# Optimization experiments

Hardware: AMD Instinct MI355X
Metric: run time of the kernel (lower is better)

## Reference

```python
import jax, jax.numpy as jnp
import numpy as np

DIM_IN = 256
DIM_OUT = 256
HEADS = 4
B, H, W = 8, 64, 64
S_Q, S_KV = 1, 2
EPS = 1e-5


def _dw_proj(x, dw, g, bta, mu, var, pw, stride):
    # depthwise 3x3 conv (groups=C) + BatchNorm (inference) + 1x1 pointwise conv
    C = x.shape[1]
    y = jax.lax.conv_general_dilated(
        x, dw, (stride, stride), [(1, 1), (1, 1)],
        dimension_numbers=('NCHW', 'OIHW', 'NCHW'), feature_group_count=C)
    inv = g / jnp.sqrt(var + EPS)
    y = (y - mu[None, :, None, None]) * inv[None, :, None, None] + bta[None, :, None, None]
    return jnp.einsum('bchw,oc->bohw', y, pw)


def setup_inputs() -> dict:
    key = jax.random.key(0)
    ks = jax.random.split(key, 16)
    f = lambda k, s: jax.random.normal(k, s, jnp.float32) * 0.05
    inp = {'x': jax.random.normal(ks[0], (B, DIM_IN, H, W), jnp.float32)}
    for i, nm in enumerate(['q', 'k', 'v']):
        inp[f'dw_{nm}'] = f(ks[1 + i], (DIM_IN, 1, 3, 3))
        inp[f'g_{nm}'] = jnp.ones((DIM_IN,), jnp.float32)
        inp[f'b_{nm}'] = jnp.zeros((DIM_IN,), jnp.float32)
        inp[f'm_{nm}'] = f(ks[4 + i], (DIM_IN,))
        inp[f'v_{nm}'] = jax.random.uniform(ks[7 + i], (DIM_IN,), jnp.float32, 0.5, 1.5)
        inp[f'pw_{nm}'] = f(ks[10 + i], (DIM_OUT, DIM_IN))
    inp['proj_w'] = f(ks[13], (DIM_OUT, DIM_OUT))
    inp['proj_b'] = f(ks[14], (DIM_OUT,))
    return inp


def reference(x, dw_q, g_q, b_q, m_q, v_q, pw_q,
              dw_k, g_k, b_k, m_k, v_k, pw_k,
              dw_v, g_v, b_v, m_v, v_v, pw_v,
              proj_w, proj_b):
    b, _, h, w = x.shape
    d = DIM_OUT // HEADS
    q = _dw_proj(x, dw_q, g_q, b_q, m_q, v_q, pw_q, S_Q)    # [b,C,h,w]
    k = _dw_proj(x, dw_k, g_k, b_k, m_k, v_k, pw_k, S_KV)   # [b,C,h/2,w/2]
    v = _dw_proj(x, dw_v, g_v, b_v, m_v, v_v, pw_v, S_KV)

    def to_heads(t):
        bb, c, hh, ww = t.shape
        # 'b c h w -> b (h w) c' then 'b t (h d) -> b h t d' (head-major channel split)
        return t.reshape(bb, HEADS, d, hh * ww).transpose(0, 1, 3, 2)  # [b,H,t,d]

    qh, kh, vh = to_heads(q), to_heads(k), to_heads(v)
    scale = DIM_OUT ** (-0.5)  # note: scales by dim_out, not head_dim (faithful)
    attn = jax.nn.softmax(jnp.einsum('bhld,bhtd->bhlt', qh, kh) * scale, axis=-1)
    out = jnp.einsum('bhlt,bhtd->bhld', attn, vh)           # [b,H,l,d]
    # 'b h (x y) d -> b (h d) x y'
    out = out.transpose(0, 1, 3, 2).reshape(b, HEADS * d, h, w)
    out = jnp.einsum('bchw,oc->bohw', out, proj_w) + proj_b[None, :, None, None]
    return out
```

## Files before the change

kernel.cpp:

```cpp
#include <hip/hip_runtime.h>

#define B_     8
#define C_     256
#define H_     64
#define W_     64
#define HEADS_ 4
#define DH_    64
#define TQ_    4096
#define TKV_   1024
#define EPS_   1e-5f
#define SCALE_ 0.0625f

typedef __attribute__((ext_vector_type(8))) short short8;
typedef __attribute__((ext_vector_type(4))) float f32x4;

#define MFMA(a, b, c) __builtin_amdgcn_mfma_f32_16x16x32_bf16((a), (b), (c), 0, 0, 0)

static __device__ __forceinline__ unsigned short f2bf(float x) {
    unsigned u = __float_as_uint(x);
    u += 0x7fff + ((u >> 16) & 1);
    return (unsigned short)(u >> 16);
}
static __device__ __forceinline__ float bf2f(unsigned short h) {
    return __uint_as_float(((unsigned)h) << 16);
}
#define GLOAD16(gp, lp) __builtin_amdgcn_global_load_lds(                      \
    (const __attribute__((address_space(1))) void*)(gp),                       \
    (__attribute__((address_space(3))) void*)(lp), 16, 0, 0)

__global__ __launch_bounds__(256)
void w2bf4_kernel(const float* __restrict__ w0, const float* __restrict__ w1,
                  const float* __restrict__ w2, const float* __restrict__ w3,
                  unsigned short* __restrict__ h0, unsigned short* __restrict__ l0,
                  unsigned short* __restrict__ h1, unsigned short* __restrict__ l1,
                  unsigned short* __restrict__ h2, unsigned short* __restrict__ l2,
                  unsigned short* __restrict__ h3, unsigned short* __restrict__ l3) {
    int m = blockIdx.y;
    const float* wm = (m == 0) ? w0 : (m == 1) ? w1 : (m == 2) ? w2 : w3;
    unsigned short* whi = (m == 0) ? h0 : (m == 1) ? h1 : (m == 2) ? h2 : h3;
    unsigned short* wlo = (m == 0) ? l0 : (m == 1) ? l1 : (m == 2) ? l2 : l3;
    int idx = (blockIdx.x * 256 + threadIdx.x) * 4;
    const float4 v4 = *(const float4*)&wm[idx];
    float vv[4] = {v4.x, v4.y, v4.z, v4.w};
    unsigned short hh[4], ll[4];
    #pragma unroll
    for (int j = 0; j < 4; ++j) { hh[j] = f2bf(vv[j]); ll[j] = f2bf(vv[j] - bf2f(hh[j])); }
    *(ushort4*)&whi[idx] = make_ushort4(hh[0], hh[1], hh[2], hh[3]);
    *(ushort4*)&wlo[idx] = make_ushort4(ll[0], ll[1], ll[2], ll[3]);
}

__global__ __launch_bounds__(256)
void dwbn3_kernel(const float* __restrict__ x,
                  const float* __restrict__ dwq, const float* __restrict__ gq,
                  const float* __restrict__ bq,  const float* __restrict__ mq,
                  const float* __restrict__ vq,  float* __restrict__ yq,
                  const float* __restrict__ dwk, const float* __restrict__ gk,
                  const float* __restrict__ bk,  const float* __restrict__ mk,
                  const float* __restrict__ vk,  float* __restrict__ yk,
                  const float* __restrict__ dwv, const float* __restrict__ gv,
                  const float* __restrict__ bv,  const float* __restrict__ mv,
                  const float* __restrict__ vv,  float* __restrict__ yv) {
    int bid = blockIdx.x;
    const float *dw, *g, *bet, *mu, *var;
    float* y;
    int stride, Ho, Wo, base;
    if (bid < 32768) {
        dw = dwq; g = gq; bet = bq; mu = mq; var = vq; y = yq;
        stride = 1; Ho = 64; Wo = 64; base = 0;
    } else if (bid < 40960) {
        dw = dwk; g = gk; bet = bk; mu = mk; var = vk; y = yk;
        stride = 2; Ho = 32; Wo = 32; base = 32768;
    } else {
        dw = dwv; g = gv; bet = bv; mu = mv; var = vv; y = yv;
        stride = 2; Ho = 32; Wo = 32; base = 40960;
    }
    int idx = (bid - base) * 256 + threadIdx.x;
    int ow = idx % Wo;
    int t  = idx / Wo;
    int oh = t % Ho; t /= Ho;
    int c  = t % C_;
    int b  = t / C_;
    const float* xp = x + ((size_t)(b * C_ + c)) * H_ * W_;
    const float* wp = dw + c * 9;
    int ih0 = oh * stride - 1, iw0 = ow * stride - 1;
    float acc = 0.f;
    #pragma unroll
    for (int kh = 0; kh < 3; ++kh) {
        int ih = ih0 + kh;
        if (ih < 0 || ih >= H_) continue;
        #pragma unroll
        for (int kw = 0; kw < 3; ++kw) {
            int iw = iw0 + kw;
            if (iw < 0 || iw >= W_) continue;
            acc = fmaf(xp[ih * W_ + iw], wp[kh * 3 + kw], acc);
        }
    }
    float inv = g[c] * __frsqrt_rn(var[c] + EPS_);
    y[idx] = (acc - mu[c]) * inv + bet[c];
}

template<int IN_BF16, int OUT_MODE>
__global__ __launch_bounds__(256, 2)
void pw_mfma(const unsigned short* __restrict__ whi, const unsigned short* __restrict__ wlo,
             const float* __restrict__ yf32,
             const unsigned short* __restrict__ yhi, const unsigned short* __restrict__ ylo,
             unsigned short* __restrict__ ohi, unsigned short* __restrict__ olo,
             float* __restrict__ of32, const float* __restrict__ bias, int Np) {
    __shared__ unsigned short Ah[64 * 64], Al[64 * 64];
    __shared__ unsigned short Bh[64 * 64], Bl[64 * 64];
    __shared__ float scr[64 * 64];

    const int tid = threadIdx.x;
    const int l = tid & 63, w = tid >> 6;
    const int g = l >> 4, ln = l & 15;
    const int pbase = blockIdx.x * 64;
    const int obase = blockIdx.y * 64;
    const int b = blockIdx.z;

    f32x4 acc[4];
    #pragma unroll
    for (int f = 0; f < 4; ++f) acc[f] = (f32x4){0.f, 0.f, 0.f, 0.f};

    for (int c0 = 0; c0 < C_; c0 += 64) {
        #pragma unroll
        for (int ii = 0; ii < 4; ++ii) {
            int ch = w * 4 + ii;
            const unsigned short* src = (ch < 8) ? whi : wlo;
            unsigned short* dst = (ch < 8) ? Ah : Al;
            int i = ch & 7;
            size_t ge = (size_t)(obase + i * 8 + (l >> 3)) * C_ + c0 +
                        (((l & 7) ^ ((l >> 3) & 7)) * 8);
            GLOAD16(src + ge, dst + i * 512);
        }
        if constexpr (IN_BF16) {
            #pragma unroll
            for (int ii = 0; ii < 4; ++ii) {
                int ch = w * 4 + ii;
                const unsigned short* src = (ch < 8) ? yhi : ylo;
                unsigned short* dst = (ch < 8) ? Bh : Bl;
                int i = ch & 7;
                size_t ge = ((size_t)b * Np + pbase + i * 8 + (l >> 3)) * C_ + c0 +
                            (((l & 7) ^ ((l >> 3) & 7)) * 8);
                GLOAD16(src + ge, dst + i * 512);
            }
        } else {
            #pragma unroll
            for (int pass = 0; pass < 4; ++pass) {
                int idx = tid + pass * 256;
                int cr = idx >> 4, p4 = (idx & 15) * 4;
                *(float4*)&scr[cr * 64 + p4] =
                    *(const float4*)&yf32[(size_t)b * C_ * Np + (size_t)(c0 + cr) * Np + pbase + p4];
            }
        }
        __syncthreads();
        if constexpr (!IN_BF16) {
            int p = tid & 63, cq = tid >> 6;
            #pragma unroll
            for (int jj = 0; jj < 4; ++jj) {
                unsigned short hh[4], ll[4];
                #pragma unroll
                for (int j = 0; j < 4; ++j) {
                    float v = scr[(cq * 16 + jj * 4 + j) * 64 + p];
                    hh[j] = f2bf(v); ll[j] = f2bf(v - bf2f(hh[j]));
                }
                int cl = cq * 16 + jj * 4;
                int e = p * 64 + (((cl >> 3) ^ (p & 7)) * 8) + (cl & 7);
                *(ushort4*)&Bh[e] = make_ushort4(hh[0], hh[1], hh[2], hh[3]);
                *(ushort4*)&Bl[e] = make_ushort4(ll[0], ll[1], ll[2], ll[3]);
            }
            __syncthreads();
        }
        #pragma unroll
        for (int kh = 0; kh < 2; ++kh) {
            int gc = kh * 4 + g;
            int ea = (16 * w + ln) * 64 + ((gc ^ (ln & 7)) * 8);
            short8 ah = *(const short8*)&Ah[ea];
            short8 al = *(const short8*)&Al[ea];
            #pragma unroll
            for (int f = 0; f < 4; ++f) {
                int p = f * 16 + ln;
                int eb = p * 64 + ((gc ^ (p & 7)) * 8);
                short8 bh = *(const short8*)&Bh[eb];
                short8 bl = *(const short8*)&Bl[eb];
                acc[f] = MFMA(ah, bh, acc[f]);
                acc[f] = MFMA(ah, bl, acc[f]);
                acc[f] = MFMA(al, bh, acc[f]);
            }
        }
        __syncthreads();
    }

    if constexpr (OUT_MODE == 0) {
        #pragma unroll
        for (int f = 0; f < 4; ++f) {
            int p = f * 16 + ln;
            #pragma unroll
            for (int r = 0; r < 4; ++r) {
                int o = 16 * w + 4 * g + r;
                scr[p * 64 + (o ^ (4 * (p & 7)))] = acc[f][r];
            }
        }
        __syncthreads();
        int p = tid & 63, oq = tid >> 6;
        #pragma unroll
        for (int jj = 0; jj < 4; ++jj) {
            unsigned short hh[4], ll[4];
            #pragma unroll
            for (int j = 0; j < 4; ++j) {
                float v = scr[p * 64 + ((oq * 16 + jj * 4 + j) ^ (4 * (p & 7)))];
                hh[j] = f2bf(v); ll[j] = f2bf(v - bf2f(hh[j]));
            }
            size_t ge = ((size_t)b * Np + pbase + p) * C_ + obase + oq * 16 + jj * 4;
            *(ushort4*)&ohi[ge] = make_ushort4(hh[0], hh[1], hh[2], hh[3]);
            *(ushort4*)&olo[ge] = make_ushort4(ll[0], ll[1], ll[2], ll[3]);
        }
    } else if constexpr (OUT_MODE == 1) {
        #pragma unroll
        for (int f = 0; f < 4; ++f) {
            int p = pbase + f * 16 + ln;
            #pragma unroll
            for (int r = 0; r < 4; ++r) {
                int o = obase + 16 * w + 4 * g + r;
                size_t ge = ((size_t)b * C_ + o) * Np + p;
                float v = acc[f][r];
                unsigned short hh = f2bf(v);
                ohi[ge] = hh; olo[ge] = f2bf(v - bf2f(hh));
            }
        }
    } else {
        float bv[4];
        #pragma unroll
        for (int r = 0; r < 4; ++r) bv[r] = bias[obase + 16 * w + 4 * g + r];
        #pragma unroll
        for (int f = 0; f < 4; ++f) {
            int p = pbase + f * 16 + ln;
            #pragma unroll
            for (int r = 0; r < 4; ++r) {
                int o = obase + 16 * w + 4 * g + r;
                of32[((size_t)b * C_ + o) * Np + p] = acc[f][r] + bv[r];
            }
        }
    }
}

__global__ __launch_bounds__(256, 2)
void attn_mfma(const unsigned short* __restrict__ qhi, const unsigned short* __restrict__ qlo,
               const unsigned short* __restrict__ khi, const unsigned short* __restrict__ klo,
               const unsigned short* __restrict__ vhi, const unsigned short* __restrict__ vlo,
               unsigned short* __restrict__ ohi, unsigned short* __restrict__ olo) {
    __shared__ unsigned short Kh[64 * 64], Kl[64 * 64];
    __shared__ unsigned short Vh[64 * 64], Vl[64 * 64];
    __shared__ unsigned short Ph[64 * 64], Pl[64 * 64];

    const int tid = threadIdx.x, l = tid & 63, w = tid >> 6;
    const int g = l >> 4, ln = l & 15;
    const int qbase = blockIdx.x * 64;
    const int h = blockIdx.y, b = blockIdx.z;

    short8 qh[2], ql[2];
    {
        size_t base = ((size_t)b * TQ_ + qbase + 16 * w + ln) * C_ + h * DH_ + g * 8;
        qh[0] = *(const short8*)&qhi[base];
        qh[1] = *(const short8*)&qhi[base + 32];
        ql[0] = *(const short8*)&qlo[base];
        ql[1] = *(const short8*)&qlo[base + 32];
    }
    f32x4 oacc[4];
    float m_run[4], l_run[4];
    #pragma unroll
    for (int f = 0; f < 4; ++f) oacc[f] = (f32x4){0.f, 0.f, 0.f, 0.f};
    #pragma unroll
    for (int r = 0; r < 4; ++r) { m_run[r] = -1e30f; l_run[r] = 0.f; }

    for (int kt = 0; kt < TKV_; kt += 64) {
        {
            const unsigned short* src = (w == 0) ? khi : (w == 1) ? klo : (w == 2) ? vhi : vlo;
            unsigned short* dst = (w == 0) ? Kh : (w == 1) ? Kl : (w == 2) ? Vh : Vl;
            int swz = ((l & 7) ^ ((l >> 3) & 7)) * 8;
            if (w < 2) {
                size_t base = ((size_t)b * TKV_ + kt) * C_ + h * DH_;
                #pragma unroll
                for (int i = 0; i < 8; ++i)
                    GLOAD16(src + base + (size_t)(i * 8 + (l >> 3)) * C_ + swz, dst + i * 512);
            } else {
                size_t base = ((size_t)b * C_ + h * DH_) * TKV_ + kt;
                #pragma unroll
                for (int i = 0; i < 8; ++i)
                    GLOAD16(src + base + (size_t)(i * 8 + (l >> 3)) * TKV_ + swz, dst + i * 512);
            }
        }
        __syncthreads();

        f32x4 sacc[4];
        #pragma unroll
        for (int f = 0; f < 4; ++f) sacc[f] = (f32x4){0.f, 0.f, 0.f, 0.f};
        #pragma unroll
        for (int kh = 0; kh < 2; ++kh) {
            #pragma unroll
            for (int f = 0; f < 4; ++f) {
                int row = f * 16 + ln;
                int e = row * 64 + (((g + 4 * kh) ^ (ln & 7)) * 8);
                short8 bh = *(const short8*)&Kh[e];
                short8 bl = *(const short8*)&Kl[e];
                sacc[f] = MFMA(qh[kh], bh, sacc[f]);
                sacc[f] = MFMA(qh[kh], bl, sacc[f]);
                sacc[f] = MFMA(ql[kh], bh, sacc[f]);
            }
        }
        #pragma unroll
        for (int r = 0; r < 4; ++r) {
            float mm = fmaxf(fmaxf(sacc[0][r], sacc[1][r]), fmaxf(sacc[2][r], sacc[3][r]));
            #pragma unroll
            for (int off = 1; off < 16; off <<= 1) mm = fmaxf(mm, __shfl_xor(mm, off, 16));
            float mnew = fmaxf(m_run[r], mm * SCALE_);
            float corr = __expf(m_run[r] - mnew);
            float pv[4], rs = 0.f;
            #pragma unroll
            for (int f = 0; f < 4; ++f) { pv[f] = __expf(sacc[f][r] * SCALE_ - mnew); rs += pv[f]; }
            #pragma unroll
            for (int off = 1; off < 16; off <<= 1) rs += __shfl_xor(rs, off, 16);
            l_run[r] = l_run[r] * corr + rs;
            m_run[r] = mnew;
            #pragma unroll
            for (int f = 0; f < 4; ++f) oacc[f][r] *= corr;
            int q = 16 * w + 4 * g + r;
            #pragma unroll
            for (int f = 0; f < 4; ++f) {
                unsigned short hh = f2bf(pv[f]);
                int e = q * 64 + (((f * 2 + (ln >> 3)) ^ (q & 7)) * 8) + (ln & 7);
                Ph[e] = hh;
                Pl[e] = f2bf(pv[f] - bf2f(hh));
            }
        }
        __syncthreads();

        #pragma unroll
        for (int kvh = 0; kvh < 2; ++kvh) {
            int qr = 16 * w + ln;
            int pe = qr * 64 + (((kvh * 4 + g) ^ (qr & 7)) * 8);
            short8 ph = *(const short8*)&Ph[pe];
            short8 pl = *(const short8*)&Pl[pe];
            #pragma unroll
            for (int f = 0; f < 4; ++f) {
                int row = f * 16 + ln;
                int e = row * 64 + (((g + 4 * kvh) ^ (ln & 7)) * 8);
                short8 bh = *(const short8*)&Vh[e];
                short8 bl = *(const short8*)&Vl[e];
                oacc[f] = MFMA(ph, bh, oacc[f]);
                oacc[f] = MFMA(ph, bl, oacc[f]);
                oacc[f] = MFMA(pl, bh, oacc[f]);
            }
        }
        __syncthreads();
    }

    float inv[4];
    #pragma unroll
    for (int r = 0; r < 4; ++r) inv[r] = 1.f / l_run[r];
    #pragma unroll
    for (int f = 0; f < 4; ++f) {
        #pragma unroll
        for (int r = 0; r < 4; ++r) {
            float v = oacc[f][r] * inv[r];
            size_t ge = ((size_t)b * TQ_ + qbase + 16 * w + 4 * g + r) * C_ + h * DH_ + f * 16 + ln;
            unsigned short hh = f2bf(v);
            ohi[ge] = hh; olo[ge] = f2bf(v - bf2f(hh));
        }
    }
}

extern "C" void kernel_launch(void* const* d_in, const int* in_sizes, int n_in,
                              void* d_out, int out_size, void* d_ws, size_t ws_size,
                              hipStream_t stream) {
    const float* x     = (const float*)d_in[0];
    const float* dw_q  = (const float*)d_in[1];
    const float* g_q   = (const float*)d_in[2];
    const float* b_q   = (const float*)d_in[3];
    const float* m_q   = (const float*)d_in[4];
    const float* v_q   = (const float*)d_in[5];
    const float* pw_q  = (const float*)d_in[6];
    const float* dw_k  = (const float*)d_in[7];
    const float* g_k   = (const float*)d_in[8];
    const float* b_k   = (const float*)d_in[9];
    const float* m_k   = (const float*)d_in[10];
    const float* v_k   = (const float*)d_in[11];
    const float* pw_k  = (const float*)d_in[12];
    const float* dw_v  = (const float*)d_in[13];
    const float* g_v   = (const float*)d_in[14];
    const float* b_v   = (const float*)d_in[15];
    const float* m_v   = (const float*)d_in[16];
    const float* v_v   = (const float*)d_in[17];
    const float* pw_v  = (const float*)d_in[18];
    const float* projw = (const float*)d_in[19];
    const float* projb = (const float*)d_in[20];
    float* out = (float*)d_out;

    const size_t NQ = (size_t)B_ * TQ_ * C_;
    const size_t NK = (size_t)B_ * TKV_ * C_;
    const size_t NW = (size_t)C_ * C_;
    char* wsb = (char*)d_ws;
    float* yq = (float*)wsb;
    unsigned short* o_hi = (unsigned short*)wsb;
    unsigned short* o_lo = o_hi + NQ;
    size_t off = NQ * 4;
    float* yk = (float*)(wsb + off); off += NK * 4;
    float* yv = (float*)(wsb + off); off += NK * 4;
    unsigned short* q_hi = (unsigned short*)(wsb + off); off += NQ * 2;
    unsigned short* q_lo = (unsigned short*)(wsb + off); off += NQ * 2;
    unsigned short* k_hi = (unsigned short*)(wsb + off); off += NK * 2;
    unsigned short* k_lo = (unsigned short*)(wsb + off); off += NK * 2;
    unsigned short* v_hi = (unsigned short*)(wsb + off); off += NK * 2;
    unsigned short* v_lo = (unsigned short*)(wsb + off); off += NK * 2;
    unsigned short* wq_hi = (unsigned short*)(wsb + off); off += NW * 2;
    unsigned short* wq_lo = (unsigned short*)(wsb + off); off += NW * 2;
    unsigned short* wk_hi = (unsigned short*)(wsb + off); off += NW * 2;
    unsigned short* wk_lo = (unsigned short*)(wsb + off); off += NW * 2;
    unsigned short* wv_hi = (unsigned short*)(wsb + off); off += NW * 2;
    unsigned short* wv_lo = (unsigned short*)(wsb + off); off += NW * 2;
    unsigned short* wp_hi = (unsigned short*)(wsb + off); off += NW * 2;
    unsigned short* wp_lo = (unsigned short*)(wsb + off); off += NW * 2;

    w2bf4_kernel<<<dim3(64, 4), 256, 0, stream>>>(
        pw_q, pw_k, pw_v, projw,
        wq_hi, wq_lo, wk_hi, wk_lo, wv_hi, wv_lo, wp_hi, wp_lo);
    dwbn3_kernel<<<49152, 256, 0, stream>>>(
        x,
        dw_q, g_q, b_q, m_q, v_q, yq,
        dw_k, g_k, b_k, m_k, v_k, yk,
        dw_v, g_v, b_v, m_v, v_v, yv);
    pw_mfma<0, 0><<<dim3(TQ_ / 64, 4, B_), 256, 0, stream>>>(
        wq_hi, wq_lo, yq, nullptr, nullptr, q_hi, q_lo, nullptr, nullptr, TQ_);
    pw_mfma<0, 0><<<dim3(TKV_ / 64, 4, B_), 256, 0, stream>>>(
        wk_hi, wk_lo, yk, nullptr, nullptr, k_hi, k_lo, nullptr, nullptr, TKV_);
    pw_mfma<0, 1><<<dim3(TKV_ / 64, 4, B_), 256, 0, stream>>>(
        wv_hi, wv_lo, yv, nullptr, nullptr, v_hi, v_lo, nullptr, nullptr, TKV_);
    attn_mfma<<<dim3(TQ_ / 64, HEADS_, B_), 256, 0, stream>>>(
        q_hi, q_lo, k_hi, k_lo, v_hi, v_lo, o_hi, o_lo);
    pw_mfma<1, 2><<<dim3(TQ_ / 64, 4, B_), 256, 0, stream>>>(
        wp_hi, wp_lo, nullptr, o_hi, o_lo, nullptr, nullptr, out, projb, TQ_);
}
```

Measured before the change: 424.2 us.

## Double-buffer K/V tiles in attention and skip softmax rescale below a threshold

The attention kernel now double-buffers the K/V LDS tiles. It issues the async global-to-LDS load of the next tile right after the barrier, so the copy overlaps with the current tile's MFMA work, and it drops the trailing per-iteration barrier. The online softmax only rescales the running max and accumulators when some row's new tile max exceeds the stored max by more than a threshold, decided per 16-lane group with a ballot. The per-row sum is kept per lane and reduced by shuffles once at the end, instead of on every tile. The price is double the K/V LDS footprint, which may limit occupancy, plus unnormalised exponentials that can reach about e^8 before a rescale.

```diff
diff --git a/kernel.cpp b/kernel.cpp
--- a/kernel.cpp
+++ b/kernel.cpp
@@ -10,6 +10,7 @@
 #define TKV_   1024
 #define EPS_   1e-5f
 #define SCALE_ 0.0625f
+#define THR_   8.0f
 
 typedef __attribute__((ext_vector_type(8))) short short8;
 typedef __attribute__((ext_vector_type(4))) float f32x4;
@@ -248,8 +249,8 @@
                const unsigned short* __restrict__ khi, const unsigned short* __restrict__ klo,
                const unsigned short* __restrict__ vhi, const unsigned short* __restrict__ vlo,
                unsigned short* __restrict__ ohi, unsigned short* __restrict__ olo) {
-    __shared__ unsigned short Kh[64 * 64], Kl[64 * 64];
-    __shared__ unsigned short Vh[64 * 64], Vl[64 * 64];
+    __shared__ unsigned short Kh[2 * 64 * 64], Kl[2 * 64 * 64];
+    __shared__ unsigned short Vh[2 * 64 * 64], Vl[2 * 64 * 64];
     __shared__ unsigned short Ph[64 * 64], Pl[64 * 64];
 
     const int tid = threadIdx.x, l = tid & 63, w = tid >> 6;
@@ -266,30 +267,32 @@
         ql[1] = *(const short8*)&qlo[base + 32];
     }
     f32x4 oacc[4];
-    float m_run[4], l_run[4];
+    float m_run[4], lpart[4];
     #pragma unroll
     for (int f = 0; f < 4; ++f) oacc[f] = (f32x4){0.f, 0.f, 0.f, 0.f};
     #pragma unroll
-    for (int r = 0; r < 4; ++r) { m_run[r] = -1e30f; l_run[r] = 0.f; }
-
-    for (int kt = 0; kt < TKV_; kt += 64) {
-        {
-            const unsigned short* src = (w == 0) ? khi : (w == 1) ? klo : (w == 2) ? vhi : vlo;
-            unsigned short* dst = (w == 0) ? Kh : (w == 1) ? Kl : (w == 2) ? Vh : Vl;
-            int swz = ((l & 7) ^ ((l >> 3) & 7)) * 8;
-            if (w < 2) {
-                size_t base = ((size_t)b * TKV_ + kt) * C_ + h * DH_;
-                #pragma unroll
-                for (int i = 0; i < 8; ++i)
-                    GLOAD16(src + base + (size_t)(i * 8 + (l >> 3)) * C_ + swz, dst + i * 512);
-            } else {
-                size_t base = ((size_t)b * C_ + h * DH_) * TKV_ + kt;
-                #pragma unroll
-                for (int i = 0; i < 8; ++i)
-                    GLOAD16(src + base + (size_t)(i * 8 + (l >> 3)) * TKV_ + swz, dst + i * 512);
-            }
-        }
+    for (int r = 0; r < 4; ++r) { m_run[r] = -1e30f; lpart[r] = 0.f; }
+
+    const int swz = ((l & 7) ^ ((l >> 3) & 7)) * 8;
+    const unsigned short* ssrc = (w == 0) ? khi : (w == 1) ? klo : (w == 2) ? vhi : vlo;
+    unsigned short* sdst0 = (w == 0) ? Kh : (w == 1) ? Kl : (w == 2) ? Vh : Vl;
+    const size_t sstride = (w < 2) ? (size_t)C_ : (size_t)TKV_;
+    const size_t sgbase  = (w < 2) ? ((size_t)b * TKV_) * C_ + h * DH_
+                                   : ((size_t)b * C_ + h * DH_) * TKV_;
+    auto STAGE = [&](int sel, int kt) {
+        size_t ko = (w < 2) ? (size_t)kt * C_ : (size_t)kt;
+        unsigned short* dst = sdst0 + sel * 4096;
+        #pragma unroll
+        for (int i = 0; i < 8; ++i)
+            GLOAD16(ssrc + sgbase + ko + (size_t)(i * 8 + (l >> 3)) * sstride + swz,
+                    dst + i * 512);
+    };
+
+    STAGE(0, 0);
+    for (int it = 0; it < TKV_ / 64; ++it) {
+        const int cur = it & 1, so = cur * 4096;
         __syncthreads();
+        if (it + 1 < TKV_ / 64) STAGE(cur ^ 1, (it + 1) * 64);
 
         f32x4 sacc[4];
         #pragma unroll
@@ -299,7 +302,7 @@
             #pragma unroll
             for (int f = 0; f < 4; ++f) {
                 int row = f * 16 + ln;
-                int e = row * 64 + (((g + 4 * kh) ^ (ln & 7)) * 8);
+                int e = so + row * 64 + (((g + 4 * kh) ^ (ln & 7)) * 8);
                 short8 bh = *(const short8*)&Kh[e];
                 short8 bl = *(const short8*)&Kl[e];
                 sacc[f] = MFMA(qh[kh], bh, sacc[f]);
@@ -307,29 +310,42 @@
                 sacc[f] = MFMA(ql[kh], bh, sacc[f]);
             }
         }
+
+        float pmax[4];
+        bool allc = true;
         #pragma unroll
         for (int r = 0; r < 4; ++r) {
             float mm = fmaxf(fmaxf(sacc[0][r], sacc[1][r]), fmaxf(sacc[2][r], sacc[3][r]));
-            #pragma unroll
-            for (int off = 1; off < 16; off <<= 1) mm = fmaxf(mm, __shfl_xor(mm, off, 16));
-            float mnew = fmaxf(m_run[r], mm * SCALE_);
-            float corr = __expf(m_run[r] - mnew);
-            float pv[4], rs = 0.f;
-            #pragma unroll
-            for (int f = 0; f < 4; ++f) { pv[f] = __expf(sacc[f][r] * SCALE_ - mnew); rs += pv[f]; }
-            #pragma unroll
-            for (int off = 1; off < 16; off <<= 1) rs += __shfl_xor(rs, off, 16);
-            l_run[r] = l_run[r] * corr + rs;
-            m_run[r] = mnew;
-            #pragma unroll
-            for (int f = 0; f < 4; ++f) oacc[f][r] *= corr;
+            pmax[r] = mm * SCALE_;
+            allc = allc && (pmax[r] <= m_run[r] + THR_);
+        }
+        unsigned long long bb = __ballot(allc);
+        bool fast = (((bb >> (g * 16)) & 0xFFFFull) == 0xFFFFull);
+        if (!fast) {
+            #pragma unroll
+            for (int r = 0; r < 4; ++r) {
+                float mm = pmax[r];
+                #pragma unroll
+                for (int off = 1; off < 16; off <<= 1) mm = fmaxf(mm, __shfl_xor(mm, off, 16));
+                float mnew = fmaxf(m_run[r], mm);
+                float corr = __expf(m_run[r] - mnew);
+                m_run[r] = mnew;
+                lpart[r] *= corr;
+                #pragma unroll
+                for (int f = 0; f < 4; ++f) oacc[f][r] *= corr;
+            }
+        }
+        #pragma unroll
+        for (int r = 0; r < 4; ++r) {
             int q = 16 * w + 4 * g + r;
             #pragma unroll
             for (int f = 0; f < 4; ++f) {
-                unsigned short hh = f2bf(pv[f]);
+                float pv = __expf(fmaf(sacc[f][r], SCALE_, -m_run[r]));
+                lpart[r] += pv;
+                unsigned short hh = f2bf(pv);
                 int e = q * 64 + (((f * 2 + (ln >> 3)) ^ (q & 7)) * 8) + (ln & 7);
                 Ph[e] = hh;
-                Pl[e] = f2bf(pv[f] - bf2f(hh));
+                Pl[e] = f2bf(pv - bf2f(hh));
             }
         }
         __syncthreads();
@@ -343,7 +359,7 @@
             #pragma unroll
             for (int f = 0; f < 4; ++f) {
                 int row = f * 16 + ln;
-                int e = row * 64 + (((g + 4 * kvh) ^ (ln & 7)) * 8);
+                int e = so + row * 64 + (((g + 4 * kvh) ^ (ln & 7)) * 8);
                 short8 bh = *(const short8*)&Vh[e];
                 short8 bl = *(const short8*)&Vl[e];
                 oacc[f] = MFMA(ph, bh, oacc[f]);
@@ -351,12 +367,16 @@
                 oacc[f] = MFMA(pl, bh, oacc[f]);
             }
         }
-        __syncthreads();
     }
 
     float inv[4];
     #pragma unroll
-    for (int r = 0; r < 4; ++r) inv[r] = 1.f / l_run[r];
+    for (int r = 0; r < 4; ++r) {
+        float s = lpart[r];
+        #pragma unroll
+        for (int off = 1; off < 16; off <<= 1) s += __shfl_xor(s, off, 16);
+        inv[r] = 1.f / s;
+    }
     #pragma unroll
     for (int f = 0; f < 4; ++f) {
         #pragma unroll
```

After: 411.7 us. 1.03x faster.
